# Kernel optimization log

Hardware: AMD Instinct MI355X
Metric: run time of the kernel (lower is better)

The kernel has to match this reference:

```python
import jax, jax.numpy as jnp
import numpy as np
from jax import lax

N_ITERS = 50  # fixed-point iteration count from the original solver


def setup_inputs() -> dict:
    key = jax.random.key(0)
    ks = jax.random.split(key, 6)
    n, n_F, p, m = 2048, 2048, 512, 512
    # Scale A, A_F so spectral radius ~0.5 (circular law: eig(randn/sqrt(n)) in unit disk)
    # -> fixed-point Sylvester iteration is contractive, matching the solver's assumption.
    A = 0.5 * jax.random.normal(ks[0], (n, n), jnp.float32) / np.sqrt(n)
    A_F = 0.5 * jax.random.normal(ks[1], (n_F, n_F), jnp.float32) / np.sqrt(n_F)
    C = jax.random.normal(ks[2], (p, n), jnp.float32) / np.sqrt(n)
    C_F = jax.random.normal(ks[3], (p, n_F), jnp.float32) / np.sqrt(n_F)
    B_F = jax.random.normal(ks[4], (n_F, m), jnp.float32) / np.sqrt(n_F)
    D_F = jax.random.normal(ks[5], (p, m), jnp.float32)
    return {"C": C, "A": A, "A_F": A_F, "B_F": B_F, "C_F": C_F, "D_F": D_F}


def _fixed_point(L, R, RHS):
    # X_{k+1} = L @ X_k @ R + RHS, X_0 = 0, run to the solver's 50-iter cap.
    # (Original breaks early when ||X_{k+1}-X_k|| < 1e-10; since the map is a
    # contraction, running the full 50 iterations yields the same fixed point.)
    def step(X, _):
        return L @ X @ R + RHS, None
    X, _ = lax.scan(step, jnp.zeros_like(RHS), None, length=N_ITERS)
    return X


def reference(C, A, A_F, B_F, C_F, D_F):
    n = A.shape[0]
    p = C.shape[0]
    m = B_F.shape[1]
    # Q12 solves A_F^H Q12 A + C_F^H C = Q12 (real inputs: conj().T == .T)
    Q12 = _fixed_point(A_F.T, A, C_F.T @ C)  # (n_F, n)
    B_hat = -(Q12.T @ B_F)  # (n, m)
    # Note: the original also solves for P12 (A P12 A_F^H + B_hat B_F^H = P12),
    # but P12 does not contribute to the returned (B_hat, D_hat); omitted (XLA
    # would dead-code-eliminate it anyway).
    # D_hat branch (n > 1): Q = I so Q_inv = I; nu = 1.
    I_n = jnp.eye(n, dtype=A.dtype)
    inv_term = jnp.linalg.inv(I_n - A.T)  # (I - nu * A^H)^{-1}
    D_lossless = jnp.eye(p, dtype=A.dtype) - C @ inv_term @ C.T  # (p, p)
    alpha = 0.5
    D_hat = alpha * (D_lossless @ jnp.ones((p, m), A.dtype)) / p + (1.0 - alpha) * D_F
    return B_hat, D_hat
```

## Files before the change

kernel.cpp:

```cpp
#include <hip/hip_runtime.h>

typedef unsigned short u16;
typedef __attribute__((ext_vector_type(4))) float f32x4;
typedef __attribute__((ext_vector_type(8))) short bf16x8;

#define AS1 __attribute__((address_space(1)))
#define AS3 __attribute__((address_space(3)))

__device__ __forceinline__ float bf2f(u16 u) {
  union { unsigned int i; float f; } v; v.i = ((unsigned int)u) << 16; return v.f;
}
__device__ __forceinline__ u16 f2bf(float f) {
  union { float f; unsigned int i; } v; v.f = f;
  unsigned int r = v.i + 0x7fffu + ((v.i >> 16) & 1u);
  return (u16)(r >> 16);
}
__device__ __forceinline__ void gload16(const void* g, void* l) {
  __builtin_amdgcn_global_load_lds((const AS1 unsigned int*)g, (AS3 unsigned int*)l, 16, 0, 0);
}

struct GemmDesc {
  const u16* A;
  const u16* Bt;
  u16* D;
  u16* Dt;
  float* Df;
  int M, N, K, lda, ldb, ldd, lddt, tn, tiles;
  float scale;
};
struct GemmBatch { GemmDesc d[4]; int nd; };

template<int BM, int BN, int FM, int FN>
__device__ __forceinline__ void epilogue(const GemmDesc& d, f32x4 (&acc)[FM][FN],
                                         int m0, int n0, int wm, int wn, int lane) {
  const int r4 = (lane >> 4) << 2;
  const int cc = lane & 15;
  #pragma unroll
  for (int i = 0; i < FM; ++i) {
    #pragma unroll
    for (int j = 0; j < FN; ++j) {
      const int row0 = m0 + wm * (BM / 2) + i * 16 + r4;
      const int col = n0 + wn * (BN / 2) + j * 16 + cc;
      float v[4];
      #pragma unroll
      for (int q = 0; q < 4; ++q) v[q] = acc[i][j][q];
      if (d.scale != 1.0f) {
        #pragma unroll
        for (int q = 0; q < 4; ++q) v[q] *= d.scale;
      }
      if (d.D) {
        #pragma unroll
        for (int q = 0; q < 4; ++q) d.D[(size_t)(row0 + q) * d.ldd + col] = f2bf(v[q]);
      }
      if (d.Df) {
        #pragma unroll
        for (int q = 0; q < 4; ++q) d.Df[(size_t)(row0 + q) * d.ldd + col] = v[q];
      }
      if (d.Dt) {
        ushort4 pk = make_ushort4(f2bf(v[0]), f2bf(v[1]), f2bf(v[2]), f2bf(v[3]));
        *(ushort4*)&d.Dt[(size_t)col * d.lddt + row0] = pk;
      }
    }
  }
}

template<int BM, int BN>
__global__ __launch_bounds__(256) void gemm_db(GemmBatch b) {
  const int nwg = gridDim.x;
  int t = ((blockIdx.x & 7) * (nwg >> 3)) + (blockIdx.x >> 3);
  int di = 0;
  while (di + 1 < b.nd && t >= b.d[di].tiles) { t -= b.d[di].tiles; ++di; }
  const GemmDesc d = b.d[di];
  const int tm = t / d.tn, tnn = t - tm * d.tn;
  const int m0 = tm * BM, n0 = tnn * BN;
  const int lane = threadIdx.x & 63;
  const int w = threadIdx.x >> 6;
  const int wm = w >> 1, wn = w & 1;
  constexpr int FM = BM / 32, FN = BN / 32;
  constexpr int HB = (BM + BN) * 64;
  __shared__ __align__(16) u16 lds[5 * HB];
  f32x4 acc[FM][FN];
  #pragma unroll
  for (int i = 0; i < FM; ++i)
    #pragma unroll
    for (int j = 0; j < FN; ++j)
      acc[i][j] = (f32x4){0.f, 0.f, 0.f, 0.f};
  const int srow = lane >> 3;
  const int scolz = (((lane & 7) << 3) ^ (srow << 3));
  const int rsw = (lane & 7) << 3;
  const int nt = d.K / 64;

  auto stagef = [&](int tt, int buf) {
    const int k0 = tt * 64;
    u16* base = &lds[buf * HB];
    #pragma unroll
    for (int c = w; c < BM / 8; c += 4)
      gload16(d.A + (size_t)(m0 + c * 8 + srow) * d.lda + k0 + scolz, base + c * 512);
    #pragma unroll
    for (int c = w; c < BN / 8; c += 4)
      gload16(d.Bt + (size_t)(n0 + c * 8 + srow) * d.ldb + k0 + scolz, base + BM * 64 + c * 512);
  };

  stagef(0, 0);
  stagef(1, 1);
  stagef(2, 2);
  stagef(3, 3);
  stagef(4, 4);
  __builtin_amdgcn_sched_barrier(0);
  asm volatile("s_waitcnt vmcnt(24)");
  __builtin_amdgcn_s_barrier();
  __builtin_amdgcn_sched_barrier(0);

  int cur = 0;
  for (int tt = 0; tt < nt; ++tt) {
    const u16* base = &lds[cur * HB];
    #pragma unroll
    for (int kk = 0; kk < 64; kk += 32) {
      const int cb = (kk + ((lane >> 4) << 3)) ^ rsw;
      bf16x8 af[FM], bfr[FN];
      #pragma unroll
      for (int i = 0; i < FM; ++i)
        af[i] = *(const bf16x8*)&base[(wm * (BM / 2) + i * 16 + (lane & 15)) * 64 + cb];
      #pragma unroll
      for (int j = 0; j < FN; ++j)
        bfr[j] = *(const bf16x8*)&base[BM * 64 + (wn * (BN / 2) + j * 16 + (lane & 15)) * 64 + cb];
      #pragma unroll
      for (int i = 0; i < FM; ++i)
        #pragma unroll
        for (int j = 0; j < FN; ++j)
          acc[i][j] = __builtin_amdgcn_mfma_f32_16x16x32_bf16(af[i], bfr[j], acc[i][j], 0, 0, 0);
    }
    if (tt + 1 < nt) {
      __builtin_amdgcn_s_barrier();
      __builtin_amdgcn_sched_barrier(0);
      if (tt + 5 < nt) {
        stagef(tt + 5, cur);
        __builtin_amdgcn_sched_barrier(0);
        asm volatile("s_waitcnt vmcnt(24)");
      } else if (tt + 4 < nt) {
        asm volatile("s_waitcnt vmcnt(18)");
      } else if (tt + 3 < nt) {
        asm volatile("s_waitcnt vmcnt(12)");
      } else if (tt + 2 < nt) {
        asm volatile("s_waitcnt vmcnt(6)");
      } else {
        asm volatile("s_waitcnt vmcnt(0)");
      }
      __builtin_amdgcn_s_barrier();
      __builtin_amdgcn_sched_barrier(0);
    }
    cur = (cur == 4) ? 0 : cur + 1;
  }
  epilogue<BM, BN, FM, FN>(d, acc, m0, n0, wm, wn, lane);
}

__global__ __launch_bounds__(256) void conv_all(const float* Af, const float* AFf,
                                                const float* Cf, const float* BFf,
                                                const float* CFf,
                                                u16* Mb, u16* Nb, u16* NbT, u16* Cb,
                                                u16* KP, u16* BFT, u16* CFb) {
  __shared__ float tile[64][65];
  const int tid = threadIdx.x;
  const int lr = tid >> 6, lc = tid & 63;
  for (int u = blockIdx.x; u < 2688; u += 1344) {
    __syncthreads();
    if (u < 1024) {
      int tr = u >> 5, tc = u & 31;
      int r0 = tr << 6, c0 = tc << 6;
      #pragma unroll
      for (int p = 0; p < 16; ++p) {
        int r = p * 4 + lr;
        tile[r][lc] = Af[(size_t)(r0 + r) * 2048 + c0 + lc];
      }
      __syncthreads();
      #pragma unroll
      for (int p = 0; p < 16; ++p) {
        int r = p * 4 + lr;
        Mb[(size_t)(c0 + r) * 2048 + r0 + lc] = f2bf(tile[lc][r]);
      }
    } else if (u < 2048) {
      int bb = u - 1024;
      int tr = bb >> 5, tc = bb & 31;
      int r0 = tr << 6, c0 = tc << 6;
      #pragma unroll
      for (int p = 0; p < 16; ++p) {
        int r = p * 4 + lr;
        float v = AFf[(size_t)(r0 + r) * 2048 + c0 + lc];
        tile[r][lc] = v;
        Nb[(size_t)(r0 + r) * 2048 + c0 + lc] = f2bf(v);
      }
      __syncthreads();
      #pragma unroll
      for (int p = 0; p < 16; ++p) {
        int r = p * 4 + lr;
        NbT[(size_t)(c0 + r) * 2048 + r0 + lc] = f2bf(tile[lc][r]);
      }
    } else if (u < 2304) {
      int bb = u - 2048;
      int tr = bb >> 5, tc = bb & 31;
      int r0 = tr << 6, c0 = tc << 6;
      #pragma unroll
      for (int p = 0; p < 16; ++p) {
        int r = p * 4 + lr;
        float v = Cf[(size_t)(r0 + r) * 2048 + c0 + lc];
        tile[r][lc] = v;
        Cb[(size_t)(r0 + r) * 2048 + c0 + lc] = f2bf(v);
      }
      __syncthreads();
      #pragma unroll
      for (int p = 0; p < 16; ++p) {
        int r = p * 4 + lr;
        KP[(size_t)(c0 + r) * 2048 + r0 + lc] = f2bf(tile[lc][r]);
      }
    } else if (u < 2560) {
      int bb = u - 2304;
      int tr = bb >> 3, tc = bb & 7;
      int r0 = tr << 6, c0 = tc << 6;
      #pragma unroll
      for (int p = 0; p < 16; ++p) {
        int r = p * 4 + lr;
        tile[r][lc] = BFf[(size_t)(r0 + r) * 512 + c0 + lc];
      }
      __syncthreads();
      #pragma unroll
      for (int p = 0; p < 16; ++p) {
        int r = p * 4 + lr;
        BFT[(size_t)(c0 + r) * 2048 + r0 + lc] = f2bf(tile[lc][r]);
      }
    } else {
      const int n4 = (512 * 2048) / 4;
      for (int i = (u - 2560) * 256 + tid; i < n4; i += 128 * 256) {
        float4 f = ((const float4*)CFf)[i];
        ((ushort4*)CFb)[i] = make_ushort4(f2bf(f.x), f2bf(f.y), f2bf(f.z), f2bf(f.w));
      }
    }
  }
}

__global__ __launch_bounds__(256) void rowsum_bf(const u16* KP, float* t, int width) {
  int w = threadIdx.x >> 6, lane = threadIdx.x & 63;
  int row = blockIdx.x * 4 + w;
  float s = 0.f;
  for (int k0 = lane * 8; k0 < width; k0 += 512) {
    bf16x8 mv = *(const bf16x8*)&KP[(size_t)row * width + k0];
    #pragma unroll
    for (int e = 0; e < 8; ++e) s += bf2f((u16)mv[e]);
  }
  #pragma unroll
  for (int off = 32; off > 0; off >>= 1) s += __shfl_down(s, off);
  if (lane == 0) t[row] = s;
}

__global__ __launch_bounds__(256) void matvec_dhat(const float* Cm, const float* t,
                                                   const float* DF, float* out) {
  __shared__ float ts[2048];
  for (int i = threadIdx.x; i < 2048; i += 256) ts[i] = t[i];
  __syncthreads();
  int w = threadIdx.x >> 6, lane = threadIdx.x & 63;
  int row = blockIdx.x * 4 + w;
  float s = 0.f;
  for (int k0 = lane * 4; k0 < 2048; k0 += 256) {
    float4 c4 = *(const float4*)&Cm[(size_t)row * 2048 + k0];
    s += c4.x * ts[k0] + c4.y * ts[k0 + 1] + c4.z * ts[k0 + 2] + c4.w * ts[k0 + 3];
  }
  #pragma unroll
  for (int off = 32; off > 0; off >>= 1) s += __shfl_down(s, off);
  s = __shfl(s, 0);
  float coef = 0.5f * (1.0f - s) * (1.0f / 512.0f);
  int j = lane * 8;
  #pragma unroll
  for (int e = 0; e < 8; ++e)
    out[(size_t)row * 512 + j + e] = coef + 0.5f * DF[(size_t)row * 512 + j + e];
}

extern "C" void kernel_launch(void* const* d_in, const int* in_sizes, int n_in,
                              void* d_out, int out_size, void* d_ws, size_t ws_size,
                              hipStream_t stream) {
  (void)in_sizes; (void)n_in; (void)out_size; (void)ws_size;
  const float* Cf  = (const float*)d_in[0];
  const float* Af  = (const float*)d_in[1];
  const float* AFf = (const float*)d_in[2];
  const float* BFf = (const float*)d_in[3];
  const float* CFf = (const float*)d_in[4];
  const float* DFf = (const float*)d_in[5];
  float* out = (float*)d_out;

  const size_t NN = 2048ull * 2048ull;
  const size_t SK = 512ull * 2048ull;
  char* ws = (char*)d_ws;
  u16* Mb   = (u16*)ws;
  u16* Nb   = Mb + NN;
  u16* NbT  = Nb + NN;
  u16* KP   = NbT + NN;
  u16* Cb   = KP + NN;
  u16* P1T  = Cb + SK;
  u16* P2T  = P1T + SK;
  u16* BFT  = P2T + SK;
  u16* E1T  = BFT + SK;
  u16* E2T  = E1T + SK;
  u16* R1   = E2T + SK;
  u16* WB   = R1 + SK;
  u16* CFb  = WB + SK;
  float* tv = (float*)(CFb + SK);

  auto mk = [](const u16* A, int lda, const u16* Bt, int ldb,
               u16* D, u16* Dt, float* Df, int ldd, int lddt,
               int M, int N, int K, float scale, int bm, int bn) {
    GemmDesc g; g.A = A; g.Bt = Bt; g.D = D; g.Dt = Dt; g.Df = Df;
    g.M = M; g.N = N; g.K = K; g.lda = lda; g.ldb = ldb; g.ldd = ldd; g.lddt = lddt;
    g.tn = N / bn; g.tiles = (M / bm) * (N / bn); g.scale = scale; return g;
  };

  conv_all<<<1344, 256, 0, stream>>>(Af, AFf, Cf, BFf, CFf, Mb, Nb, NbT, Cb, KP, BFT, CFb);

  { GemmBatch gb{}; gb.nd = 2;
    gb.d[0] = mk(Mb, 2048, Cb, 2048, KP + 512, P1T, nullptr, 2048, 2048, 2048, 512, 2048, 1.f, 128, 64);
    gb.d[1] = mk(Nb, 2048, BFT, 2048, nullptr, E1T, nullptr, 0, 2048, 2048, 512, 2048, 1.f, 128, 64);
    gemm_db<128, 64><<<256, 256, 0, stream>>>(gb); }

  { GemmBatch gb{}; gb.nd = 2;
    gb.d[0] = mk(Mb, 2048, P1T, 2048, KP + 1024, P2T, nullptr, 2048, 2048, 2048, 512, 2048, 1.f, 128, 64);
    gb.d[1] = mk(CFb, 2048, NbT, 2048, R1, nullptr, nullptr, 2048, 0, 512, 2048, 2048, 1.f, 128, 64);
    gemm_db<128, 64><<<256, 256, 0, stream>>>(gb); }

  { GemmBatch gb{}; gb.nd = 2;
    gb.d[0] = mk(Mb, 2048, P2T, 2048, KP + 1536, nullptr, nullptr, 2048, 0, 2048, 512, 2048, 1.f, 128, 64);
    gb.d[1] = mk(Nb, 2048, E1T, 2048, nullptr, E2T, nullptr, 0, 2048, 2048, 512, 2048, 1.f, 128, 64);
    gemm_db<128, 64><<<256, 256, 0, stream>>>(gb); }

  { GemmBatch gb{}; gb.nd = 4;
    gb.d[0] = mk(CFb, 2048, BFT, 2048, nullptr, WB, nullptr, 0, 2048, 512, 512, 2048, 1.f, 128, 64);
    gb.d[1] = mk(CFb, 2048, E1T, 2048, nullptr, WB + 512, nullptr, 0, 2048, 512, 512, 2048, 1.f, 128, 64);
    gb.d[2] = mk(R1, 2048, E1T, 2048, nullptr, WB + 1024, nullptr, 0, 2048, 512, 512, 2048, 1.f, 128, 64);
    gb.d[3] = mk(R1, 2048, E2T, 2048, nullptr, WB + 1536, nullptr, 0, 2048, 512, 512, 2048, 1.f, 128, 64);
    gemm_db<128, 64><<<128, 256, 0, stream>>>(gb); }

  { GemmBatch gb{}; gb.nd = 1;
    gb.d[0] = mk(KP, 2048, WB, 2048, nullptr, nullptr, out, 512, 0, 2048, 512, 2048, -1.f, 128, 64);
    gemm_db<128, 64><<<128, 256, 0, stream>>>(gb); }

  rowsum_bf<<<512, 256, 0, stream>>>(KP, tv, 2048);
  matvec_dhat<<<128, 256, 0, stream>>>(Cf, tv, DFf, out + 2048 * 512);
}
```

Before: 137.1 us.

## Split-K the last two GEMM stages and restage pipeline as 2-deep 128-wide K tiles

The final two GEMM launches ran only 128 workgroups, so they are split along K into two halves, doubling the workgroup count to 256. Small elementwise kernels then add the partial results, applying the negation for the output. The shared GEMM kernel's LDS pipeline also changes from five 64-wide K stages to two double-buffered 128-wide stages with a matching vmcnt wait. This adds two extra launches, extra partial-result traffic, and an extra bf16 rounding of WB, and the shallower prefetch may expose more load latency in the other GEMMs.

```diff
diff --git a/kernel.cpp b/kernel.cpp
--- a/kernel.cpp
+++ b/kernel.cpp
@@ -28,7 +28,7 @@
   int M, N, K, lda, ldb, ldd, lddt, tn, tiles;
   float scale;
 };
-struct GemmBatch { GemmDesc d[4]; int nd; };
+struct GemmBatch { GemmDesc d[8]; int nd; };
 
 template<int BM, int BN, int FM, int FN>
 __device__ __forceinline__ void epilogue(const GemmDesc& d, f32x4 (&acc)[FM][FN],
@@ -78,7 +78,8 @@
   const int wm = w >> 1, wn = w & 1;
   constexpr int FM = BM / 32, FN = BN / 32;
   constexpr int HB = (BM + BN) * 64;
-  __shared__ __align__(16) u16 lds[5 * HB];
+  constexpr int L = 2 * (BM + BN) / 32;
+  __shared__ __align__(16) u16 lds[4 * HB];
   f32x4 acc[FM][FN];
   #pragma unroll
   for (int i = 0; i < FM; ++i)
@@ -88,68 +89,63 @@
   const int srow = lane >> 3;
   const int scolz = (((lane & 7) << 3) ^ (srow << 3));
   const int rsw = (lane & 7) << 3;
-  const int nt = d.K / 64;
+  const int nt = d.K / 128;
 
   auto stagef = [&](int tt, int buf) {
-    const int k0 = tt * 64;
-    u16* base = &lds[buf * HB];
-    #pragma unroll
-    for (int c = w; c < BM / 8; c += 4)
-      gload16(d.A + (size_t)(m0 + c * 8 + srow) * d.lda + k0 + scolz, base + c * 512);
-    #pragma unroll
-    for (int c = w; c < BN / 8; c += 4)
-      gload16(d.Bt + (size_t)(n0 + c * 8 + srow) * d.ldb + k0 + scolz, base + BM * 64 + c * 512);
+    #pragma unroll
+    for (int h = 0; h < 2; ++h) {
+      const int k0 = tt * 128 + h * 64;
+      u16* base = &lds[(buf * 2 + h) * HB];
+      #pragma unroll
+      for (int c = w; c < BM / 8; c += 4)
+        gload16(d.A + (size_t)(m0 + c * 8 + srow) * d.lda + k0 + scolz, base + c * 512);
+      #pragma unroll
+      for (int c = w; c < BN / 8; c += 4)
+        gload16(d.Bt + (size_t)(n0 + c * 8 + srow) * d.ldb + k0 + scolz, base + BM * 64 + c * 512);
+    }
   };
 
   stagef(0, 0);
   stagef(1, 1);
-  stagef(2, 2);
-  stagef(3, 3);
-  stagef(4, 4);
   __builtin_amdgcn_sched_barrier(0);
-  asm volatile("s_waitcnt vmcnt(24)");
+  asm volatile("s_waitcnt vmcnt(%0)" :: "n"(L));
   __builtin_amdgcn_s_barrier();
   __builtin_amdgcn_sched_barrier(0);
 
-  int cur = 0;
   for (int tt = 0; tt < nt; ++tt) {
-    const u16* base = &lds[cur * HB];
-    #pragma unroll
-    for (int kk = 0; kk < 64; kk += 32) {
-      const int cb = (kk + ((lane >> 4) << 3)) ^ rsw;
-      bf16x8 af[FM], bfr[FN];
-      #pragma unroll
-      for (int i = 0; i < FM; ++i)
-        af[i] = *(const bf16x8*)&base[(wm * (BM / 2) + i * 16 + (lane & 15)) * 64 + cb];
-      #pragma unroll
-      for (int j = 0; j < FN; ++j)
-        bfr[j] = *(const bf16x8*)&base[BM * 64 + (wn * (BN / 2) + j * 16 + (lane & 15)) * 64 + cb];
-      #pragma unroll
-      for (int i = 0; i < FM; ++i)
+    #pragma unroll
+    for (int h = 0; h < 2; ++h) {
+      const u16* base = &lds[((tt & 1) * 2 + h) * HB];
+      #pragma unroll
+      for (int kk = 0; kk < 64; kk += 32) {
+        const int cb = (kk + ((lane >> 4) << 3)) ^ rsw;
+        bf16x8 af[FM], bfr[FN];
+        #pragma unroll
+        for (int i = 0; i < FM; ++i)
+          af[i] = *(const bf16x8*)&base[(wm * (BM / 2) + i * 16 + (lane & 15)) * 64 + cb];
         #pragma unroll
         for (int j = 0; j < FN; ++j)
-          acc[i][j] = __builtin_amdgcn_mfma_f32_16x16x32_bf16(af[i], bfr[j], acc[i][j], 0, 0, 0);
+          bfr[j] = *(const bf16x8*)&base[BM * 64 + (wn * (BN / 2) + j * 16 + (lane & 15)) * 64 + cb];
+        #pragma unroll
+        for (int i = 0; i < FM; ++i)
+          #pragma unroll
+          for (int j = 0; j < FN; ++j)
+            acc[i][j] = __builtin_amdgcn_mfma_f32_16x16x32_bf16(af[i], bfr[j], acc[i][j], 0, 0, 0);
+      }
     }
     if (tt + 1 < nt) {
       __builtin_amdgcn_s_barrier();
       __builtin_amdgcn_sched_barrier(0);
-      if (tt + 5 < nt) {
-        stagef(tt + 5, cur);
+      if (tt + 2 < nt) {
+        stagef(tt + 2, tt & 1);
         __builtin_amdgcn_sched_barrier(0);
-        asm volatile("s_waitcnt vmcnt(24)");
-      } else if (tt + 4 < nt) {
-        asm volatile("s_waitcnt vmcnt(18)");
-      } else if (tt + 3 < nt) {
-        asm volatile("s_waitcnt vmcnt(12)");
-      } else if (tt + 2 < nt) {
-        asm volatile("s_waitcnt vmcnt(6)");
+        asm volatile("s_waitcnt vmcnt(%0)" :: "n"(L));
       } else {
         asm volatile("s_waitcnt vmcnt(0)");
       }
       __builtin_amdgcn_s_barrier();
       __builtin_amdgcn_sched_barrier(0);
     }
-    cur = (cur == 4) ? 0 : cur + 1;
   }
   epilogue<BM, BN, FM, FN>(d, acc, m0, n0, wm, wn, lane);
 }
@@ -235,6 +231,27 @@
       }
     }
   }
+}
+
+__global__ __launch_bounds__(256) void comb_wb(const u16* a, const u16* b, u16* o, int n4) {
+  int i = blockIdx.x * 256 + threadIdx.x;
+  if (i >= n4) return;
+  ushort4 x = ((const ushort4*)a)[i];
+  ushort4 y = ((const ushort4*)b)[i];
+  ushort4 r;
+  r.x = f2bf(bf2f(x.x) + bf2f(y.x));
+  r.y = f2bf(bf2f(x.y) + bf2f(y.y));
+  r.z = f2bf(bf2f(x.z) + bf2f(y.z));
+  r.w = f2bf(bf2f(x.w) + bf2f(y.w));
+  ((ushort4*)o)[i] = r;
+}
+
+__global__ __launch_bounds__(256) void comb_out(const float* a, const float* b, float* o, int n4) {
+  int i = blockIdx.x * 256 + threadIdx.x;
+  if (i >= n4) return;
+  float4 x = ((const float4*)a)[i];
+  float4 y = ((const float4*)b)[i];
+  ((float4*)o)[i] = make_float4(-(x.x + y.x), -(x.y + y.y), -(x.z + y.z), -(x.w + y.w));
 }
 
 __global__ __launch_bounds__(256) void rowsum_bf(const u16* KP, float* t, int width) {
@@ -300,8 +317,12 @@
   u16* E2T  = E1T + SK;
   u16* R1   = E2T + SK;
   u16* WB   = R1 + SK;
-  u16* CFb  = WB + SK;
-  float* tv = (float*)(CFb + SK);
+  u16* WBp0 = WB + SK;
+  u16* WBp1 = WBp0 + SK;
+  u16* CFb  = WBp1 + SK;
+  float* Vp0 = (float*)(CFb + SK);
+  float* Vp1 = Vp0 + 2048ull * 512;
+  float* tv  = Vp1 + 2048ull * 512;
 
   auto mk = [](const u16* A, int lda, const u16* Bt, int ldb,
                u16* D, u16* Dt, float* Df, int ldd, int lddt,
@@ -328,16 +349,22 @@
     gb.d[1] = mk(Nb, 2048, E1T, 2048, nullptr, E2T, nullptr, 0, 2048, 2048, 512, 2048, 1.f, 128, 64);
     gemm_db<128, 64><<<256, 256, 0, stream>>>(gb); }
 
-  { GemmBatch gb{}; gb.nd = 4;
-    gb.d[0] = mk(CFb, 2048, BFT, 2048, nullptr, WB, nullptr, 0, 2048, 512, 512, 2048, 1.f, 128, 64);
-    gb.d[1] = mk(CFb, 2048, E1T, 2048, nullptr, WB + 512, nullptr, 0, 2048, 512, 512, 2048, 1.f, 128, 64);
-    gb.d[2] = mk(R1, 2048, E1T, 2048, nullptr, WB + 1024, nullptr, 0, 2048, 512, 512, 2048, 1.f, 128, 64);
-    gb.d[3] = mk(R1, 2048, E2T, 2048, nullptr, WB + 1536, nullptr, 0, 2048, 512, 512, 2048, 1.f, 128, 64);
-    gemm_db<128, 64><<<128, 256, 0, stream>>>(gb); }
-
-  { GemmBatch gb{}; gb.nd = 1;
-    gb.d[0] = mk(KP, 2048, WB, 2048, nullptr, nullptr, out, 512, 0, 2048, 512, 2048, -1.f, 128, 64);
-    gemm_db<128, 64><<<128, 256, 0, stream>>>(gb); }
+  { GemmBatch gb{}; gb.nd = 8;
+    const u16* As[4] = {CFb, CFb, R1, R1};
+    const u16* Bs[4] = {BFT, E1T, E1T, E2T};
+    for (int k = 0; k < 4; ++k)
+      for (int h = 0; h < 2; ++h)
+        gb.d[k * 2 + h] = mk(As[k] + h * 1024, 2048, Bs[k] + h * 1024, 2048,
+                             nullptr, (h ? WBp1 : WBp0) + 512 * k, nullptr, 0, 2048,
+                             512, 512, 1024, 1.f, 128, 64);
+    gemm_db<128, 64><<<256, 256, 0, stream>>>(gb); }
+  comb_wb<<<1024, 256, 0, stream>>>(WBp0, WBp1, WB, (512 * 2048) / 4);
+
+  { GemmBatch gb{}; gb.nd = 2;
+    gb.d[0] = mk(KP, 2048, WB, 2048, nullptr, nullptr, Vp0, 512, 0, 2048, 512, 1024, 1.f, 128, 64);
+    gb.d[1] = mk(KP + 1024, 2048, WB + 1024, 2048, nullptr, nullptr, Vp1, 512, 0, 2048, 512, 1024, 1.f, 128, 64);
+    gemm_db<128, 64><<<256, 256, 0, stream>>>(gb); }
+  comb_out<<<1024, 256, 0, stream>>>(Vp0, Vp1, out, (2048 * 512) / 4);
 
   rowsum_bf<<<512, 256, 0, stream>>>(KP, tv, 2048);
   matvec_dhat<<<128, 256, 0, stream>>>(Cf, tv, DFf, out + 2048 * 512);
```

Result: faster. 117.6 us (-14.2%).
